# Performance work log

Hardware: AMD Instinct MI355X
Metric: run time of the kernel (lower is better)

The kernel has to match this reference:

```python
import jax, jax.numpy as jnp
import numpy as np


def setup_inputs() -> dict:
    key = jax.random.key(0)
    k1, k2 = jax.random.split(key)
    N, M, D = 8192, 8192, 64
    X1 = jax.random.normal(k1, (N, D), dtype=jnp.float32)
    X2 = jax.random.normal(k2, (M, D), dtype=jnp.float32)
    l = jnp.float32(1.0)
    sigma_f = jnp.float32(1.0)
    return {"X1": X1, "X2": X2, "l": l, "sigma_f": sigma_f}


def reference(X1, X2, l, sigma_f):
    sq1 = jnp.sum(X1 * X1, axis=1)               # [N]
    sq2 = jnp.sum(X2 * X2, axis=1)               # [M]
    cross = jnp.einsum("nd,md->nm", X1, X2)      # [N,M] GEMM
    dist = sq1[:, None] + sq2[None, :] - 2.0 * cross
    dist = jnp.maximum(dist, 0.0)                # clamp numerical negatives
    return sigma_f ** 2 * jnp.exp(-0.5 * dist / l ** 2)
```

## Files before the change

### kernel.cpp

```cpp
#include <hip/hip_runtime.h>
#include <hip/hip_bf16.h>

#define DD 64
#define TN 64
#define TM 128

typedef short short8 __attribute__((ext_vector_type(8)));
typedef unsigned short us8 __attribute__((ext_vector_type(8)));
typedef float f32x4 __attribute__((ext_vector_type(4)));

__device__ __forceinline__ float bf2f(unsigned short h) {
    union { unsigned u; float f; } v; v.u = ((unsigned)h) << 16;
    return v.f;
}
__device__ __forceinline__ unsigned short f2bf(float x) {
    __hip_bfloat16 b = __float2bfloat16(x);
    unsigned short u;
    __builtin_memcpy(&u, &b, 2);
    return u;
}

__global__ __launch_bounds__(256, 2) void sqexp_kernel(
    const float* __restrict__ X1, const float* __restrict__ X2,
    const float* __restrict__ lp, const float* __restrict__ sfp,
    float* __restrict__ out, int N, int M)
{
    __shared__ __align__(16) unsigned char Bbuf[2 * TM * DD * 2];
    __shared__ __align__(16) unsigned char Obuf[TN * TM * 4];
    __shared__ float sq1[TN];
    __shared__ float sq2[TM];

    unsigned short* Bh = (unsigned short*)Bbuf;
    unsigned short* Bl = (unsigned short*)(Bbuf + TM * DD * 2);

    const int t    = threadIdx.x;
    const int w    = t >> 6;
    const int lane = t & 63;
    const int n0   = blockIdx.y * TN;
    const int m0   = blockIdx.x * (2 * TM);

    const int wr = (w >> 1) * 32;
    const int wc = (w & 1) * 64;

    const float lv_ = lp[0], sf = sfp[0];
    const float c1  = -0.5f / (lv_ * lv_);
    const float cm2 = -2.0f * c1;
    const float amp = sf * sf;

    const int brow_ = t >> 1;
    const int bhalf = t & 1;

    auto loadB = [&](int mbase, float4 (&f)[8]) {
        const float4* Bp = (const float4*)(X2 + (size_t)(mbase + brow_) * DD) + bhalf * 8;
        #pragma unroll
        for (int j = 0; j < 8; ++j) f[j] = Bp[j];
    };
    auto writeB = [&](float4 (&f)[8]) {
        float s2 = 0.0f;
        #pragma unroll
        for (int c = 0; c < 4; ++c) {
            float4 f0 = f[2 * c], f1 = f[2 * c + 1];
            float xs[8] = { f0.x, f0.y, f0.z, f0.w, f1.x, f1.y, f1.z, f1.w };
            us8 hv, lv;
            #pragma unroll
            for (int e = 0; e < 8; ++e) {
                s2 = fmaf(xs[e], xs[e], s2);
                unsigned short h = f2bf(xs[e]);
                hv[e] = h;
                lv[e] = f2bf(xs[e] - bf2f(h));
            }
            int byte = brow_ * 128 + (((bhalf * 4 + c) * 16) ^ ((brow_ & 7) << 4));
            *(us8*)&Bh[byte >> 1] = hv;
            *(us8*)&Bl[byte >> 1] = lv;
        }
        s2 += __shfl_xor(s2, 1);
        if (bhalf == 0) sq2[brow_] = s2;
    };

    short8 ah[2][2], al[2][2];
    auto computeTile = [&](f32x4 (&acc)[2][4]) {
        #pragma unroll
        for (int ks = 0; ks < 2; ++ks) {
            #pragma unroll
            for (int fn = 0; fn < 4; ++fn) {
                int br   = wc + fn * 16 + (lane & 15);
                int byte = br * 128 + (((ks * 64) + (lane >> 4) * 16) ^ ((br & 7) << 4));
                short8 bh = *(const short8*)&Bh[byte >> 1];
                short8 bl = *(const short8*)&Bl[byte >> 1];
                #pragma unroll
                for (int fm = 0; fm < 2; ++fm) {
                    acc[fm][fn] = __builtin_amdgcn_mfma_f32_16x16x32_bf16(bh, ah[fm][ks], acc[fm][fn], 0, 0, 0);
                    acc[fm][fn] = __builtin_amdgcn_mfma_f32_16x16x32_bf16(bl, ah[fm][ks], acc[fm][fn], 0, 0, 0);
                    acc[fm][fn] = __builtin_amdgcn_mfma_f32_16x16x32_bf16(bh, al[fm][ks], acc[fm][fn], 0, 0, 0);
                }
            }
        }
    };
    auto epilogueTile = [&](f32x4 (&acc)[2][4]) {
        float a1[2];
        #pragma unroll
        for (int fm = 0; fm < 2; ++fm) a1[fm] = c1 * sq1[wr + fm * 16 + (lane & 15)];
        #pragma unroll
        for (int fn = 0; fn < 4; ++fn) {
            f32x4 s  = *(const f32x4*)&sq2[wc + fn * 16 + (lane >> 4) * 4];
            f32x4 a2 = c1 * s;
            #pragma unroll
            for (int fm = 0; fm < 2; ++fm) {
                f32x4 o;
                #pragma unroll
                for (int r = 0; r < 4; ++r) {
                    float arg = fminf(fmaf(cm2, acc[fm][fn][r], a1[fm] + a2[r]), 0.0f);
                    o[r] = amp * __expf(arg);
                }
                int R = wr + fm * 16 + (lane & 15);
                int C = wc + fn * 16 + (lane >> 4) * 4;
                *(f32x4*)(Obuf + R * 512 + ((C * 4) ^ ((R & 7) << 4))) = o;
            }
        }
    };
    auto storeTile = [&](int mbase) {
        #pragma unroll
        for (int i = 0; i < 8; ++i) {
            int R = w * 16 + i * 2 + (lane >> 5);
            int c = lane & 31;
            f32x4 v = *(const f32x4*)(Obuf + R * 512 + ((c ^ (R & 7)) * 16));
            *(f32x4*)&out[(size_t)(n0 + R) * M + mbase + 4 * c] = v;
        }
    };

    #pragma unroll
    for (int fm = 0; fm < 2; ++fm) {
        const int row = n0 + wr + fm * 16 + (lane & 15);
        const float4* Ap = (const float4*)(X1 + (size_t)row * DD) + (lane >> 4) * 2;
        float p = 0.0f;
        #pragma unroll
        for (int ks = 0; ks < 2; ++ks) {
            float4 f0 = Ap[ks * 8];
            float4 f1 = Ap[ks * 8 + 1];
            float xs[8] = { f0.x, f0.y, f0.z, f0.w, f1.x, f1.y, f1.z, f1.w };
            us8 hv, lv;
            #pragma unroll
            for (int e = 0; e < 8; ++e) {
                p = fmaf(xs[e], xs[e], p);
                unsigned short h = f2bf(xs[e]);
                hv[e] = h;
                lv[e] = f2bf(xs[e] - bf2f(h));
            }
            __builtin_memcpy(&ah[fm][ks], &hv, 16);
            __builtin_memcpy(&al[fm][ks], &lv, 16);
        }
        p += __shfl_xor(p, 16);
        p += __shfl_xor(p, 32);
        if ((w & 1) == 0 && (lane >> 4) == 0) sq1[wr + fm * 16 + lane] = p;
    }

    {
        float4 f[8];
        loadB(m0, f);
        writeB(f);
    }
    __syncthreads();

    f32x4 accA[2][4] = {};
    computeTile(accA);
    epilogueTile(accA);
    __syncthreads();

    {
        float4 f[8];
        loadB(m0 + TM, f);
        storeTile(m0);
        writeB(f);
    }
    __syncthreads();

    f32x4 accB[2][4] = {};
    computeTile(accB);
    epilogueTile(accB);
    __syncthreads();

    storeTile(m0 + TM);
}

extern "C" void kernel_launch(void* const* d_in, const int* in_sizes, int n_in,
                              void* d_out, int out_size, void* d_ws, size_t ws_size,
                              hipStream_t stream) {
    const float* X1 = (const float*)d_in[0];
    const float* X2 = (const float*)d_in[1];
    const float* lp = (const float*)d_in[2];
    const float* sf = (const float*)d_in[3];
    float* out = (float*)d_out;
    const int N = in_sizes[0] / DD;
    const int M = in_sizes[1] / DD;
    dim3 grid(M / (2 * TM), N / TN);
    sqexp_kernel<<<grid, 256, 0, stream>>>(X1, X2, lp, sf, out, N, M);
}
```

Baseline: 82.11 us.

## Keep B tile resident and loop over row tiles with per-wave output staging

Each block now loads and splits one 128-column X2 tile into bf16 hi/lo once, then loops over 8 row tiles of 128 rows. X1 loads for the next tile are prefetched into registers while the current tile computes. Each wave owns 32 rows and all 128 columns and stages its output through a private LDS region, so the per-tile block barriers are gone. This cuts redundant X2 loading and conversion and the block-level syncs. In exchange it uses more accumulators per thread (register pressure), launches fewer blocks (8*64=512), and still serializes the store behind the epilogue within each wave.

```diff
diff --git a/kernel.cpp b/kernel.cpp
--- a/kernel.cpp
+++ b/kernel.cpp
@@ -2,8 +2,9 @@
 #include <hip/hip_bf16.h>
 
 #define DD 64
-#define TN 64
 #define TM 128
+#define TROWS 128
+#define NTILES 8
 
 typedef short short8 __attribute__((ext_vector_type(8)));
 typedef unsigned short us8 __attribute__((ext_vector_type(8)));
@@ -25,9 +26,8 @@
     const float* __restrict__ lp, const float* __restrict__ sfp,
     float* __restrict__ out, int N, int M)
 {
-    __shared__ __align__(16) unsigned char Bbuf[2 * TM * DD * 2];
-    __shared__ __align__(16) unsigned char Obuf[TN * TM * 4];
-    __shared__ float sq1[TN];
+    __shared__ __align__(16) unsigned char Bbuf[TM * DD * 2 * 2];
+    __shared__ __align__(16) unsigned char Obuf[4 * 8192];
     __shared__ float sq2[TM];
 
     unsigned short* Bh = (unsigned short*)Bbuf;
@@ -36,26 +36,25 @@
     const int t    = threadIdx.x;
     const int w    = t >> 6;
     const int lane = t & 63;
-    const int n0   = blockIdx.y * TN;
-    const int m0   = blockIdx.x * (2 * TM);
 
-    const int wr = (w >> 1) * 32;
-    const int wc = (w & 1) * 64;
+    const int npx     = M / TM;
+    const int bx      = blockIdx.x % npx;
+    const int by      = blockIdx.x / npx;
+    const int m0      = bx * TM;
+    const int rowband = by * (TROWS * NTILES);
 
     const float lv_ = lp[0], sf = sfp[0];
     const float c1  = -0.5f / (lv_ * lv_);
     const float cm2 = -2.0f * c1;
     const float amp = sf * sf;
 
-    const int brow_ = t >> 1;
-    const int bhalf = t & 1;
-
-    auto loadB = [&](int mbase, float4 (&f)[8]) {
-        const float4* Bp = (const float4*)(X2 + (size_t)(mbase + brow_) * DD) + bhalf * 8;
+    {
+        const int brow = t >> 1, half = t & 1;
+        const float4* Bp = (const float4*)(X2 + (size_t)(m0 + brow) * DD) + half * 8;
+        float4 f[8];
         #pragma unroll
         for (int j = 0; j < 8; ++j) f[j] = Bp[j];
-    };
-    auto writeB = [&](float4 (&f)[8]) {
+
         float s2 = 0.0f;
         #pragma unroll
         for (int c = 0; c < 4; ++c) {
@@ -69,22 +68,69 @@
                 hv[e] = h;
                 lv[e] = f2bf(xs[e] - bf2f(h));
             }
-            int byte = brow_ * 128 + (((bhalf * 4 + c) * 16) ^ ((brow_ & 7) << 4));
+            int byte = brow * 128 + (((half * 4 + c) * 16) ^ ((brow & 7) << 4));
             *(us8*)&Bh[byte >> 1] = hv;
             *(us8*)&Bl[byte >> 1] = lv;
         }
         s2 += __shfl_xor(s2, 1);
-        if (bhalf == 0) sq2[brow_] = s2;
+        if (half == 0) sq2[brow] = s2;
+    }
+
+    float4 pre[2][2][2];
+    auto issueA = [&](int tt) {
+        #pragma unroll
+        for (int fm = 0; fm < 2; ++fm) {
+            const int row = rowband + tt * TROWS + w * 32 + fm * 16 + (lane & 15);
+            const float4* Ap = (const float4*)(X1 + (size_t)row * DD) + (lane >> 4) * 2;
+            pre[fm][0][0] = Ap[0];
+            pre[fm][0][1] = Ap[1];
+            pre[fm][1][0] = Ap[8];
+            pre[fm][1][1] = Ap[9];
+        }
+    };
+    short8 ah[2][2], al[2][2];
+    float a1[2];
+    auto convertA = [&]() {
+        #pragma unroll
+        for (int fm = 0; fm < 2; ++fm) {
+            float p = 0.0f;
+            #pragma unroll
+            for (int ks = 0; ks < 2; ++ks) {
+                float4 f0 = pre[fm][ks][0], f1 = pre[fm][ks][1];
+                float xs[8] = { f0.x, f0.y, f0.z, f0.w, f1.x, f1.y, f1.z, f1.w };
+                us8 hv, lv;
+                #pragma unroll
+                for (int e = 0; e < 8; ++e) {
+                    p = fmaf(xs[e], xs[e], p);
+                    unsigned short h = f2bf(xs[e]);
+                    hv[e] = h;
+                    lv[e] = f2bf(xs[e] - bf2f(h));
+                }
+                __builtin_memcpy(&ah[fm][ks], &hv, 16);
+                __builtin_memcpy(&al[fm][ks], &lv, 16);
+            }
+            p += __shfl_xor(p, 16);
+            p += __shfl_xor(p, 32);
+            a1[fm] = c1 * p;
+        }
     };
 
-    short8 ah[2][2], al[2][2];
-    auto computeTile = [&](f32x4 (&acc)[2][4]) {
+    issueA(0);
+    convertA();
+    __syncthreads();
+
+    unsigned char* myO = Obuf + w * 8192;
+
+    for (int tt = 0; tt < NTILES; ++tt) {
+        if (tt + 1 < NTILES) issueA(tt + 1);
+
+        f32x4 acc[2][8] = {};
         #pragma unroll
         for (int ks = 0; ks < 2; ++ks) {
             #pragma unroll
-            for (int fn = 0; fn < 4; ++fn) {
-                int br   = wc + fn * 16 + (lane & 15);
-                int byte = br * 128 + (((ks * 64) + (lane >> 4) * 16) ^ ((br & 7) << 4));
+            for (int fn = 0; fn < 8; ++fn) {
+                int brow = fn * 16 + (lane & 15);
+                int byte = brow * 128 + (((ks * 64) + (lane >> 4) * 16) ^ ((brow & 7) << 4));
                 short8 bh = *(const short8*)&Bh[byte >> 1];
                 short8 bl = *(const short8*)&Bl[byte >> 1];
                 #pragma unroll
@@ -95,91 +141,35 @@
                 }
             }
         }
-    };
-    auto epilogueTile = [&](f32x4 (&acc)[2][4]) {
-        float a1[2];
+
         #pragma unroll
-        for (int fm = 0; fm < 2; ++fm) a1[fm] = c1 * sq1[wr + fm * 16 + (lane & 15)];
-        #pragma unroll
-        for (int fn = 0; fn < 4; ++fn) {
-            f32x4 s  = *(const f32x4*)&sq2[wc + fn * 16 + (lane >> 4) * 4];
-            f32x4 a2 = c1 * s;
+        for (int fm = 0; fm < 2; ++fm) {
             #pragma unroll
-            for (int fm = 0; fm < 2; ++fm) {
+            for (int fn = 0; fn < 8; ++fn) {
+                f32x4 s  = *(const f32x4*)&sq2[fn * 16 + (lane >> 4) * 4];
+                f32x4 a2 = c1 * s;
                 f32x4 o;
                 #pragma unroll
                 for (int r = 0; r < 4; ++r) {
                     float arg = fminf(fmaf(cm2, acc[fm][fn][r], a1[fm] + a2[r]), 0.0f);
                     o[r] = amp * __expf(arg);
                 }
-                int R = wr + fm * 16 + (lane & 15);
-                int C = wc + fn * 16 + (lane >> 4) * 4;
-                *(f32x4*)(Obuf + R * 512 + ((C * 4) ^ ((R & 7) << 4))) = o;
+                int R = lane & 15;
+                int C = fn * 16 + (lane >> 4) * 4;
+                *(f32x4*)(myO + R * 512 + ((C * 4) ^ ((R & 7) << 4))) = o;
+            }
+            #pragma unroll
+            for (int i = 0; i < 8; ++i) {
+                int R = i * 2 + (lane >> 5);
+                int c = lane & 31;
+                f32x4 v = *(const f32x4*)(myO + R * 512 + ((c ^ (R & 7)) * 16));
+                size_t row = (size_t)(rowband + tt * TROWS + w * 32 + fm * 16 + R);
+                *(f32x4*)&out[row * M + m0 + 4 * c] = v;
             }
         }
-    };
-    auto storeTile = [&](int mbase) {
-        #pragma unroll
-        for (int i = 0; i < 8; ++i) {
-            int R = w * 16 + i * 2 + (lane >> 5);
-            int c = lane & 31;
-            f32x4 v = *(const f32x4*)(Obuf + R * 512 + ((c ^ (R & 7)) * 16));
-            *(f32x4*)&out[(size_t)(n0 + R) * M + mbase + 4 * c] = v;
-        }
-    };
 
-    #pragma unroll
-    for (int fm = 0; fm < 2; ++fm) {
-        const int row = n0 + wr + fm * 16 + (lane & 15);
-        const float4* Ap = (const float4*)(X1 + (size_t)row * DD) + (lane >> 4) * 2;
-        float p = 0.0f;
-        #pragma unroll
-        for (int ks = 0; ks < 2; ++ks) {
-            float4 f0 = Ap[ks * 8];
-            float4 f1 = Ap[ks * 8 + 1];
-            float xs[8] = { f0.x, f0.y, f0.z, f0.w, f1.x, f1.y, f1.z, f1.w };
-            us8 hv, lv;
-            #pragma unroll
-            for (int e = 0; e < 8; ++e) {
-                p = fmaf(xs[e], xs[e], p);
-                unsigned short h = f2bf(xs[e]);
-                hv[e] = h;
-                lv[e] = f2bf(xs[e] - bf2f(h));
-            }
-            __builtin_memcpy(&ah[fm][ks], &hv, 16);
-            __builtin_memcpy(&al[fm][ks], &lv, 16);
-        }
-        p += __shfl_xor(p, 16);
-        p += __shfl_xor(p, 32);
-        if ((w & 1) == 0 && (lane >> 4) == 0) sq1[wr + fm * 16 + lane] = p;
+        if (tt + 1 < NTILES) convertA();
     }
-
-    {
-        float4 f[8];
-        loadB(m0, f);
-        writeB(f);
-    }
-    __syncthreads();
-
-    f32x4 accA[2][4] = {};
-    computeTile(accA);
-    epilogueTile(accA);
-    __syncthreads();
-
-    {
-        float4 f[8];
-        loadB(m0 + TM, f);
-        storeTile(m0);
-        writeB(f);
-    }
-    __syncthreads();
-
-    f32x4 accB[2][4] = {};
-    computeTile(accB);
-    epilogueTile(accB);
-    __syncthreads();
-
-    storeTile(m0 + TM);
 }
 
 extern "C" void kernel_launch(void* const* d_in, const int* in_sizes, int n_in,
@@ -192,6 +182,6 @@
     float* out = (float*)d_out;
     const int N = in_sizes[0] / DD;
     const int M = in_sizes[1] / DD;
-    dim3 grid(M / (2 * TM), N / TN);
-    sqexp_kernel<<<grid, 256, 0, stream>>>(X1, X2, lp, sf, out, N, M);
+    const int nblk = (M / TM) * (N / (TROWS * NTILES));
+    sqexp_kernel<<<nblk, 256, 0, stream>>>(X1, X2, lp, sf, out, N, M);
 }
```

New measurement: 152.5 us. 1.86x slower.
